# Kernel tuning notes

Hardware: AMD Instinct MI355X
Metric: run time of the kernel (lower is better)

The kernel has to match this reference:

```python
import jax, jax.numpy as jnp
import numpy as np

N_NODES = 20000
N_EDGES = 320000
IN_CH = 512
HID = 128
HEADS = 4
OUT_CH = 30
NEG_SLOPE = 0.2  # PyG GATConv default negative_slope


def add_self_loops(ei, n):
    loops = jnp.arange(n, dtype=ei.dtype)
    return jnp.concatenate([ei, jnp.stack([loops, loops])], axis=1)


def gat_layer(x, ei, W, a_src, a_dst, b, concat):
    # x: [N, F_in], ei: [2, E] (source row 0 -> target row 1), W: [F_in, H*C]
    n = x.shape[0]
    H, C = a_src.shape
    h = (x @ W).reshape(n, H, C)                      # [N, H, C]
    src, dst = ei[0], ei[1]
    al_src = jnp.einsum('nhc,hc->nh', h, a_src)       # [N, H]
    al_dst = jnp.einsum('nhc,hc->nh', h, a_dst)
    e = al_src[src] + al_dst[dst]                     # [E, H]
    e = jnp.where(e > 0, e, NEG_SLOPE * e)            # LeakyReLU
    # segment softmax over destination nodes (stable)
    emax = jax.lax.stop_gradient(jax.ops.segment_max(e, dst, num_segments=n))
    p = jnp.exp(e - emax[dst])
    denom = jax.ops.segment_sum(p, dst, num_segments=n)
    alpha = p / denom[dst]                            # [E, H]
    msg = h[src] * alpha[:, :, None]                  # [E, H, C]
    out = jax.ops.segment_sum(msg, dst, num_segments=n)  # [N, H, C]
    out = out.reshape(n, H * C) if concat else out.mean(axis=1)
    return out + b


def setup_inputs() -> dict:
    key = jax.random.key(0)
    ks = jax.random.split(key, 12)
    s = 0.05
    x = jax.random.normal(ks[0], (N_NODES, IN_CH), jnp.float32)
    edge_index = jax.random.randint(ks[1], (2, N_EDGES), 0, N_NODES, jnp.int32)
    return {
        'x': x,
        'edge_index': edge_index,
        'W1': jax.random.normal(ks[2], (IN_CH, HEADS * HID), jnp.float32) * s,
        'a_src1': jax.random.normal(ks[3], (HEADS, HID), jnp.float32) * s,
        'a_dst1': jax.random.normal(ks[4], (HEADS, HID), jnp.float32) * s,
        'b1': jnp.zeros((HEADS * HID,), jnp.float32),
        'W2': jax.random.normal(ks[5], (HEADS * HID, OUT_CH), jnp.float32) * s,
        'a_src2': jax.random.normal(ks[6], (1, OUT_CH), jnp.float32) * s,
        'a_dst2': jax.random.normal(ks[7], (1, OUT_CH), jnp.float32) * s,
        'b2': jnp.zeros((OUT_CH,), jnp.float32),
        'Wd': jax.random.normal(ks[8], (OUT_CH, IN_CH), jnp.float32) * s,
        'bd': jnp.zeros((IN_CH,), jnp.float32),
    }


def reference(x, edge_index, W1, a_src1, a_dst1, b1, W2, a_src2, a_dst2, b2, Wd, bd):
    n = x.shape[0]
    ei = add_self_loops(edge_index, n)
    h = gat_layer(x, ei, W1, a_src1, a_dst1, b1, concat=True)   # [N, HEADS*HID]
    h = jax.nn.elu(h)                                           # dropout is identity in eval
    z = gat_layer(h, ei, W2, a_src2, a_dst2, b2, concat=False)  # [N, OUT_CH]
    x_hat = z @ Wd + bd                                         # [N, IN_CH]
    return (x_hat, z)
```

## Files before the change

kernel.cpp:

```cpp
#include <hip/hip_runtime.h>
#include <hip/hip_bf16.h>
#include <stdint.h>

#define N_NODES 20000
#define N_EDGES 320000
#define IN_CH 512
#define HID 128
#define HEADS 4
#define HC 512
#define OUT_CH 30
#define NEG_SLOPE 0.2f
#define M_PAD 20096

typedef _Float16 half8 __attribute__((ext_vector_type(8)));
typedef _Float16 half4v __attribute__((ext_vector_type(4)));
typedef float f32x4 __attribute__((ext_vector_type(4)));

static __device__ __forceinline__ float lrelu(float e) { return e > 0.f ? e : NEG_SLOPE * e; }

static __device__ __forceinline__ void gload16(const void* gsrc, void* ldst) {
  __builtin_amdgcn_global_load_lds(
      (const __attribute__((address_space(1))) uint32_t*)gsrc,
      (__attribute__((address_space(3))) uint32_t*)ldst,
      16, 0, 0);
}

__global__ __launch_bounds__(256) void k_cast_x(const float* __restrict__ x,
                                                _Float16* __restrict__ xh,
                                                int* __restrict__ cnt) {
  int i = blockIdx.x * blockDim.x + threadIdx.x;
  if (i < N_NODES) cnt[i] = 0;
  int base = i * 4;
  int row = base >> 9;
  half4v o;
  if (row < N_NODES) {
    float4 v = *(const float4*)(x + (size_t)base);
    o[0] = (_Float16)v.x; o[1] = (_Float16)v.y; o[2] = (_Float16)v.z; o[3] = (_Float16)v.w;
  } else {
    o[0] = o[1] = o[2] = o[3] = (_Float16)0.f;
  }
  *(half4v*)(xh + (size_t)base) = o;
}

__global__ __launch_bounds__(256) void k_prep_w(const float* __restrict__ W1,
                                                const float* __restrict__ W2,
                                                _Float16* __restrict__ W1t,
                                                _Float16* __restrict__ w2t) {
  __shared__ float t[64][65];
  const int b = blockIdx.x;
  const int tid = threadIdx.x;
  if (b < 64) {
    const int bk = (b & 7) * 64;
    const int bn = (b >> 3) * 64;
#pragma unroll
    for (int it = 0; it < 16; it++) {
      int idx = tid + it * 256;
      int r = idx >> 6, c = idx & 63;
      t[r][c] = W1[(size_t)(bk + r) * HC + bn + c];
    }
    __syncthreads();
#pragma unroll
    for (int it = 0; it < 16; it++) {
      int idx = tid + it * 256;
      int rn = idx >> 6, ck = idx & 63;
      W1t[(size_t)(bn + rn) * IN_CH + bk + ck] = (_Float16)t[ck][rn];
    }
  } else {
    int idx = (b - 64) * 256 + tid;
    int n = idx >> 9, k = idx & 511;
    w2t[idx] = (n < OUT_CH) ? (_Float16)W2[(size_t)k * OUT_CH + n] : (_Float16)0.f;
  }
}

__global__ __launch_bounds__(256) void k_gemm1_mfma(const _Float16* __restrict__ A,
                                                    const _Float16* __restrict__ Bt,
                                                    _Float16* __restrict__ C,
                                                    const float* __restrict__ a_src,
                                                    const float* __restrict__ a_dst,
                                                    float* __restrict__ al_s,
                                                    float* __restrict__ al_d) {
  __shared__ _Float16 smem[128 * 136];
  _Float16* As = smem;
  _Float16* Bs = smem + 128 * 64;
  _Float16* Cs = smem;
  const int tid = threadIdx.x;
  const int lane = tid & 63;
  const int w = tid >> 6;
  const int bm = blockIdx.x * 128;
  const int bn = blockIdx.y * 128;

  const int lrow = lane >> 3;
  const int schunk = (lane & 7) ^ lrow;

  const int wm = w >> 1, wn = w & 1;
  const int r15 = lane & 15;
  const int q = lane >> 4;
  const int a_row0 = wm * 64 + r15;
  const int b_row0 = wn * 64 + r15;

  f32x4 acc[4][4];
  const f32x4 zero = {0.f, 0.f, 0.f, 0.f};
#pragma unroll
  for (int i = 0; i < 4; i++)
#pragma unroll
    for (int j = 0; j < 4; j++) acc[i][j] = zero;

  for (int kb = 0; kb < 8; kb++) {
    const int kof = kb * 64 + schunk * 8;
#pragma unroll
    for (int t = 0; t < 4; t++) {
      const int row = w * 32 + t * 8;
      gload16(A + (size_t)(bm + row + lrow) * IN_CH + kof, (void*)(As + row * 64));
      gload16(Bt + (size_t)(bn + row + lrow) * IN_CH + kof, (void*)(Bs + row * 64));
    }
    __syncthreads();
#pragma unroll
    for (int s = 0; s < 2; s++) {
      const int cs = ((s * 4 + q) ^ (lane & 7)) * 8;
      half8 af[4], bf[4];
#pragma unroll
      for (int i = 0; i < 4; i++) af[i] = *(const half8*)&As[(a_row0 + i * 16) * 64 + cs];
#pragma unroll
      for (int j = 0; j < 4; j++) bf[j] = *(const half8*)&Bs[(b_row0 + j * 16) * 64 + cs];
#pragma unroll
      for (int i = 0; i < 4; i++)
#pragma unroll
        for (int j = 0; j < 4; j++)
          acc[i][j] = __builtin_amdgcn_mfma_f32_16x16x32_f16(af[i], bf[j], acc[i][j], 0, 0, 0);
    }
    __syncthreads();
  }
#pragma unroll
  for (int i = 0; i < 4; i++)
#pragma unroll
    for (int j = 0; j < 4; j++)
#pragma unroll
      for (int r = 0; r < 4; r++) {
        const int row = wm * 64 + i * 16 + q * 4 + r;
        const int col = wn * 64 + j * 16 + r15;
        Cs[row * 136 + col] = (_Float16)acc[i][j][r];
      }
  __syncthreads();
#pragma unroll
  for (int it = 0; it < 8; it++) {
    int cidx = tid + it * 256;
    int row = cidx >> 4, c16 = cidx & 15;
    int gm = bm + row;
    if (gm < N_NODES)
      *(half8*)(C + (size_t)gm * HC + bn + c16 * 8) = *(const half8*)&Cs[row * 136 + c16 * 8];
  }
  const int head = blockIdx.y;
  const int row = tid >> 1;
  const int hf = tid & 1;
  const float* asp = a_src + head * HID + hf * 64;
  const float* adp = a_dst + head * HID + hf * 64;
  float s = 0.f, d = 0.f;
#pragma unroll
  for (int j8 = 0; j8 < 8; j8++) {
    half8 cv = *(const half8*)&Cs[row * 136 + hf * 64 + j8 * 8];
    float4 a0 = *(const float4*)(asp + j8 * 8);
    float4 a1 = *(const float4*)(asp + j8 * 8 + 4);
    float4 d0 = *(const float4*)(adp + j8 * 8);
    float4 d1 = *(const float4*)(adp + j8 * 8 + 4);
    float c0 = (float)cv[0], c1 = (float)cv[1], c2 = (float)cv[2], c3 = (float)cv[3];
    float c4 = (float)cv[4], c5 = (float)cv[5], c6 = (float)cv[6], c7 = (float)cv[7];
    s += c0 * a0.x + c1 * a0.y + c2 * a0.z + c3 * a0.w +
         c4 * a1.x + c5 * a1.y + c6 * a1.z + c7 * a1.w;
    d += c0 * d0.x + c1 * d0.y + c2 * d0.z + c3 * d0.w +
         c4 * d1.x + c5 * d1.y + c6 * d1.z + c7 * d1.w;
  }
  s += __shfl_xor(s, 1);
  d += __shfl_xor(d, 1);
  const int gm = bm + row;
  if (hf == 0 && gm < N_NODES) {
    al_s[gm * HEADS + head] = s;
    al_d[gm * HEADS + head] = d;
  }
}

#define PARTS 79
__global__ void k_count(const int* __restrict__ dst, int* __restrict__ cnt) {
  int e = blockIdx.x * blockDim.x + threadIdx.x;
  if (e < N_EDGES) atomicAdd(&cnt[dst[e]], 1);
}
__global__ __launch_bounds__(256) void k_scan_part(const int* __restrict__ cnt,
                                                   int* __restrict__ part) {
  __shared__ int ws[4];
  int i = blockIdx.x * 256 + threadIdx.x;
  int v = (i < N_NODES) ? cnt[i] : 0;
  int lane = threadIdx.x & 63;
#pragma unroll
  for (int off = 32; off; off >>= 1) v += __shfl_down(v, off);
  if (lane == 0) ws[threadIdx.x >> 6] = v;
  __syncthreads();
  if (threadIdx.x == 0) part[blockIdx.x] = ws[0] + ws[1] + ws[2] + ws[3];
}
__global__ __launch_bounds__(128) void k_scan_tops(int* __restrict__ part,
                                                   int* __restrict__ offs) {
  __shared__ int buf[128];
  int t = threadIdx.x;
  int v = (t < PARTS) ? part[t] : 0;
  buf[t] = v;
  __syncthreads();
#pragma unroll
  for (int off = 1; off < 128; off <<= 1) {
    int x = (t >= off) ? buf[t - off] : 0;
    __syncthreads();
    buf[t] += x;
    __syncthreads();
  }
  if (t < PARTS) part[t] = buf[t] - v;
  if (t == PARTS - 1) offs[N_NODES] = buf[t];
}
__global__ __launch_bounds__(256) void k_scan_final(const int* __restrict__ cnt,
                                                    const int* __restrict__ part,
                                                    int* __restrict__ offs,
                                                    int* __restrict__ cursor) {
  __shared__ int buf[256];
  int i = blockIdx.x * 256 + threadIdx.x;
  int t = threadIdx.x;
  int v = (i < N_NODES) ? cnt[i] : 0;
  buf[t] = v;
  __syncthreads();
#pragma unroll
  for (int off = 1; off < 256; off <<= 1) {
    int x = (t >= off) ? buf[t - off] : 0;
    __syncthreads();
    buf[t] += x;
    __syncthreads();
  }
  if (i < N_NODES) {
    int ex = part[blockIdx.x] + buf[t] - v;
    offs[i] = ex;
    cursor[i] = ex;
  }
}
__global__ void k_scatter(const int* __restrict__ src, const int* __restrict__ dst,
                          int* __restrict__ cursor, int* __restrict__ srcs) {
  int e = blockIdx.x * blockDim.x + threadIdx.x;
  if (e < N_EDGES) {
    int pos = atomicAdd(&cursor[dst[e]], 1);
    srcs[pos] = src[e];
  }
}

__global__ __launch_bounds__(256) void k_agg1(const _Float16* __restrict__ h,
                                              const float* __restrict__ al_s,
                                              const float* __restrict__ al_d,
                                              const int* __restrict__ offs,
                                              const int* __restrict__ srcs,
                                              const float* __restrict__ b1,
                                              _Float16* __restrict__ hm) {
  const int lane = threadIdx.x & 63;
  const int qq = lane >> 4;
  const int l16 = lane & 15;
  const int head = blockIdx.x / 1250;
  const int n = (blockIdx.x % 1250) * 16 + (threadIdx.x >> 6) * 4 + qq;
  const int cb = head * HID + l16 * 8;

  const float adn = al_d[n * HEADS + head];
  const float pself = __expf(lrelu(al_s[n * HEADS + head] + adn));

  half8 hv = *(const half8*)(h + (size_t)n * HC + cb);
  float acc[8];
  float den = pself;
#pragma unroll
  for (int j = 0; j < 8; j++) acc[j] = pself * (float)hv[j];

  const int beg = offs[n];
  const int cnt = offs[n + 1] - beg;
  int mx = cnt;
  mx = max(mx, __shfl_xor(mx, 16));
  mx = max(mx, __shfl_xor(mx, 32));
  const int kb = qq * 16;

  for (int base = 0; base < mx; base += 16) {
    int sreg = n;
    float preg = 0.f;
    if (base + l16 < cnt) {
      sreg = srcs[beg + base + l16];
      preg = __expf(lrelu(al_s[sreg * HEADS + head] + adn));
    }
    int m = min(16, cnt - base);
    int m4 = (m + 3) & ~3;
    for (int k = 0; k < m4; k += 4) {
      int s0 = __shfl(sreg, kb + k);
      int s1 = __shfl(sreg, kb + k + 1);
      int s2 = __shfl(sreg, kb + k + 2);
      int s3 = __shfl(sreg, kb + k + 3);
      float p0 = __shfl(preg, kb + k);
      float p1 = __shfl(preg, kb + k + 1);
      float p2 = __shfl(preg, kb + k + 2);
      float p3 = __shfl(preg, kb + k + 3);
      half8 v0 = *(const half8*)(h + (size_t)s0 * HC + cb);
      half8 v1 = *(const half8*)(h + (size_t)s1 * HC + cb);
      half8 v2 = *(const half8*)(h + (size_t)s2 * HC + cb);
      half8 v3 = *(const half8*)(h + (size_t)s3 * HC + cb);
      den += p0 + p1 + p2 + p3;
#pragma unroll
      for (int j = 0; j < 8; j++)
        acc[j] += p0 * (float)v0[j] + p1 * (float)v1[j] +
                  p2 * (float)v2[j] + p3 * (float)v3[j];
    }
  }
  const float inv = 1.f / den;
  float4 bb0 = *(const float4*)(b1 + cb);
  float4 bb1 = *(const float4*)(b1 + cb + 4);
  float ob[8] = {bb0.x, bb0.y, bb0.z, bb0.w, bb1.x, bb1.y, bb1.z, bb1.w};
  half8 ov;
#pragma unroll
  for (int j = 0; j < 8; j++) {
    float o = acc[j] * inv + ob[j];
    o = o > 0.f ? o : __expf(o) - 1.f;
    ov[j] = (_Float16)o;
  }
  *(half8*)(hm + (size_t)n * HC + cb) = ov;
}

__global__ __launch_bounds__(256) void k_gemm2_mfma(const _Float16* __restrict__ hm,
                                                    const _Float16* __restrict__ w2t,
                                                    const float* __restrict__ a_s2,
                                                    const float* __restrict__ a_d2,
                                                    float* __restrict__ zpre,
                                                    float* __restrict__ al_s2,
                                                    float* __restrict__ al_d2) {
  __shared__ _Float16 Bs[32 * 520];
  __shared__ _Float16 As[64 * 136];
  const int tid = threadIdx.x;
  const int lane = tid & 63;
  const int w = tid >> 6;
  const int bm = blockIdx.x * 64;
  const int n15 = lane & 15;
  const int q = lane >> 4;

#pragma unroll
  for (int it = 0; it < 8; it++) {
    int idx = (tid + it * 256) * 8;
    int n = idx >> 9, k = idx & 511;
    *(half8*)&Bs[n * 520 + k] = *(const half8*)(w2t + idx);
  }

  f32x4 acc0 = {0.f, 0.f, 0.f, 0.f}, acc1 = {0.f, 0.f, 0.f, 0.f};
  for (int kt = 0; kt < HC; kt += 128) {
#pragma unroll
    for (int p = 0; p < 4; p++) {
      int row = (tid >> 4) + p * 16;
      int kof = (tid & 15) * 8;
      int gm = bm + row;
      half8 v = {};
      if (gm < N_NODES) v = *(const half8*)(hm + (size_t)gm * HC + kt + kof);
      *(half8*)&As[row * 136 + kof] = v;
    }
    __syncthreads();
#pragma unroll
    for (int ks = 0; ks < 128; ks += 32) {
      half8 af = *(const half8*)&As[(w * 16 + n15) * 136 + ks + q * 8];
      half8 b0 = *(const half8*)&Bs[n15 * 520 + kt + ks + q * 8];
      half8 b1 = *(const half8*)&Bs[(16 + n15) * 520 + kt + ks + q * 8];
      acc0 = __builtin_amdgcn_mfma_f32_16x16x32_f16(af, b0, acc0, 0, 0, 0);
      acc1 = __builtin_amdgcn_mfma_f32_16x16x32_f16(af, b1, acc1, 0, 0, 0);
    }
    __syncthreads();
  }
  const float asn0 = (n15 < OUT_CH) ? a_s2[n15] : 0.f;
  const float asn1 = (n15 + 16 < OUT_CH) ? a_s2[n15 + 16] : 0.f;
  const float adn0 = (n15 < OUT_CH) ? a_d2[n15] : 0.f;
  const float adn1 = (n15 + 16 < OUT_CH) ? a_d2[n15 + 16] : 0.f;
#pragma unroll
  for (int r = 0; r < 4; r++) {
    const int gm = bm + w * 16 + q * 4 + r;
    const bool ok = gm < N_NODES;
    if (ok) {
      zpre[(size_t)gm * OUT_CH + n15] = acc0[r];
      if (n15 + 16 < OUT_CH) zpre[(size_t)gm * OUT_CH + n15 + 16] = acc1[r];
    }
    float s = acc0[r] * asn0 + acc1[r] * asn1;
    float d = acc0[r] * adn0 + acc1[r] * adn1;
#pragma unroll
    for (int off = 8; off; off >>= 1) {
      s += __shfl_xor(s, off);
      d += __shfl_xor(d, off);
    }
    if (n15 == 0 && ok) {
      al_s2[gm] = s;
      al_d2[gm] = d;
    }
  }
}

__global__ __launch_bounds__(256) void k_agg2(const float* __restrict__ zpre,
                                              const float* __restrict__ al_s2,
                                              const float* __restrict__ al_d2,
                                              const int* __restrict__ offs,
                                              const int* __restrict__ srcs,
                                              const float* __restrict__ b2,
                                              float* __restrict__ zout) {
  const int lane = threadIdx.x & 63;
  const int hh = lane >> 5;
  const int l32 = lane & 31;
  const int n = blockIdx.x * 8 + (threadIdx.x >> 6) * 2 + hh;
  const float ad2n = al_d2[n];
  const float pself = __expf(lrelu(al_s2[n] + ad2n));
  const bool act = l32 < OUT_CH;
  float zv = act ? zpre[(size_t)n * OUT_CH + l32] : 0.f;
  float acc = pself * zv;
  float den = pself;

  const int beg = offs[n];
  const int cnt = offs[n + 1] - beg;
  int mx = max(cnt, __shfl_xor(cnt, 32));
  const int kb = hh * 32;

  for (int base = 0; base < mx; base += 32) {
    int sreg = n;
    float preg = 0.f;
    if (base + l32 < cnt) {
      sreg = srcs[beg + base + l32];
      preg = __expf(lrelu(al_s2[sreg] + ad2n));
    }
    int m = min(32, cnt - base);
    int m4 = (m + 3) & ~3;
    for (int k = 0; k < m4; k += 4) {
      int s0 = __shfl(sreg, kb + k);
      int s1 = __shfl(sreg, kb + k + 1);
      int s2 = __shfl(sreg, kb + k + 2);
      int s3 = __shfl(sreg, kb + k + 3);
      float p0 = __shfl(preg, kb + k);
      float p1 = __shfl(preg, kb + k + 1);
      float p2 = __shfl(preg, kb + k + 2);
      float p3 = __shfl(preg, kb + k + 3);
      float v0 = act ? zpre[(size_t)s0 * OUT_CH + l32] : 0.f;
      float v1 = act ? zpre[(size_t)s1 * OUT_CH + l32] : 0.f;
      float v2 = act ? zpre[(size_t)s2 * OUT_CH + l32] : 0.f;
      float v3 = act ? zpre[(size_t)s3 * OUT_CH + l32] : 0.f;
      den += p0 + p1 + p2 + p3;
      acc += p0 * v0 + p1 * v1 + p2 * v2 + p3 * v3;
    }
  }
  if (act) zout[(size_t)n * OUT_CH + l32] = acc / den + b2[l32];
}

__global__ __launch_bounds__(256) void k_dec(const float* __restrict__ z,
                                             const float* __restrict__ Wd,
                                             const float* __restrict__ bd,
                                             float* __restrict__ xhat) {
  __shared__ float zs[64][32];
  const int tid = threadIdx.x;
  const int c = blockIdx.y * 256 + tid;
  float wd[32];
#pragma unroll
  for (int k = 0; k < OUT_CH; k++) wd[k] = Wd[(size_t)k * IN_CH + c];
  wd[30] = wd[31] = 0.f;
  const int n0 = blockIdx.x * 64;
  for (int idx = tid; idx < 64 * 32; idx += 256) {
    int r = idx >> 5, cc = idx & 31;
    int row = n0 + r;
    zs[r][cc] = (cc < OUT_CH && row < N_NODES) ? z[(size_t)row * OUT_CH + cc] : 0.f;
  }
  __syncthreads();
  const float b0 = bd[c];
  for (int i = 0; i < 64; i++) {
    int row = n0 + i;
    if (row >= N_NODES) break;
    float a0 = b0;
#pragma unroll
    for (int k4 = 0; k4 < 8; k4++) {
      float4 zv = *(const float4*)&zs[i][k4 * 4];
      a0 += zv.x * wd[k4 * 4 + 0] + zv.y * wd[k4 * 4 + 1] +
            zv.z * wd[k4 * 4 + 2] + zv.w * wd[k4 * 4 + 3];
    }
    xhat[(size_t)row * IN_CH + c] = a0;
  }
}

extern "C" void kernel_launch(void* const* d_in, const int* in_sizes, int n_in,
                              void* d_out, int out_size, void* d_ws, size_t ws_size,
                              hipStream_t stream) {
  const float* x    = (const float*)d_in[0];
  const int*   ei   = (const int*)d_in[1];
  const float* W1   = (const float*)d_in[2];
  const float* a_s1 = (const float*)d_in[3];
  const float* a_d1 = (const float*)d_in[4];
  const float* b1   = (const float*)d_in[5];
  const float* W2   = (const float*)d_in[6];
  const float* a_s2 = (const float*)d_in[7];
  const float* a_d2 = (const float*)d_in[8];
  const float* b2   = (const float*)d_in[9];
  const float* Wd   = (const float*)d_in[10];
  const float* bd   = (const float*)d_in[11];

  float* xhat = (float*)d_out;
  float* zout = xhat + (size_t)N_NODES * IN_CH;

  const int* srcv = ei;
  const int* dstv = ei + N_EDGES;

  char* w = (char*)d_ws;
  auto alloc = [&](size_t bytes) {
    void* p = (void*)w;
    w += (bytes + 255) & ~(size_t)255;
    return p;
  };
  _Float16* xh   = (_Float16*)alloc((size_t)M_PAD * IN_CH * 2);
  _Float16* w1t  = (_Float16*)alloc((size_t)HC * IN_CH * 2);
  _Float16* w2t  = (_Float16*)alloc((size_t)32 * HC * 2);
  _Float16* h    = (_Float16*)alloc((size_t)N_NODES * HC * 2);
  _Float16* hm   = (_Float16*)alloc((size_t)N_NODES * HC * 2);
  float* zpre  = (float*)alloc((size_t)N_NODES * OUT_CH * 4);
  float* al_s1v= (float*)alloc((size_t)N_NODES * HEADS * 4);
  float* al_d1v= (float*)alloc((size_t)N_NODES * HEADS * 4);
  float* al_s2v= (float*)alloc((size_t)N_NODES * 4);
  float* al_d2v= (float*)alloc((size_t)N_NODES * 4);
  int*   cnt   = (int*)alloc((size_t)N_NODES * 4);
  int*   offs  = (int*)alloc((size_t)(N_NODES + 1) * 4);
  int*   cursor= (int*)alloc((size_t)N_NODES * 4);
  int*   srcs  = (int*)alloc((size_t)N_EDGES * 4);
  int*   part  = (int*)alloc((size_t)PARTS * 4);

  const int EB = (N_EDGES + 255) / 256;

  k_prep_w<<<128, 256, 0, stream>>>(W1, W2, w1t, w2t);
  k_cast_x<<<M_PAD * IN_CH / 4 / 256, 256, 0, stream>>>(x, xh, cnt);
  k_gemm1_mfma<<<dim3(M_PAD / 128, HC / 128), 256, 0, stream>>>(xh, w1t, h, a_s1, a_d1,
                                                                al_s1v, al_d1v);
  k_count<<<EB, 256, 0, stream>>>(dstv, cnt);
  k_scan_part<<<PARTS, 256, 0, stream>>>(cnt, part);
  k_scan_tops<<<1, 128, 0, stream>>>(part, offs);
  k_scan_final<<<PARTS, 256, 0, stream>>>(cnt, part, offs, cursor);
  k_scatter<<<EB, 256, 0, stream>>>(srcv, dstv, cursor, srcs);
  k_agg1<<<1250 * HEADS, 256, 0, stream>>>(h, al_s1v, al_d1v, offs, srcs, b1, hm);
  k_gemm2_mfma<<<(N_NODES + 63) / 64, 256, 0, stream>>>(hm, w2t, a_s2, a_d2, zpre,
                                                        al_s2v, al_d2v);
  k_agg2<<<N_NODES / 8, 256, 0, stream>>>(zpre, al_s2v, al_d2v, offs, srcs, b2, zout);
  k_dec<<<dim3((N_NODES + 63) / 64, 2), 256, 0, stream>>>(zout, Wd, bd, xhat);
}
```

Measured before the change: 267.0 us.

## Merge front kernels, fold edge count into GEMM1, drop scan_tops, LDS edge staging

Merges the x cast and weight prep into a single launch and appends the edge-count atomics as extra blocks of the GEMM1 grid, so both run in one dispatch. Removes the single-block top-level scan by having each final-scan block sum the earlier partials itself. In both aggregation kernels, source indices and weights are staged in LDS and read back as vector loads, replacing eight cross-lane shuffles per four edges. The goal is fewer launches and fewer serialized tiny kernels. The cost is some redundant partial summation and extra LDS traffic.

```diff
diff --git a/kernel.cpp b/kernel.cpp
--- a/kernel.cpp
+++ b/kernel.cpp
@@ -11,6 +11,10 @@
 #define OUT_CH 30
 #define NEG_SLOPE 0.2f
 #define M_PAD 20096
+#define PARTS 79
+#define CAST_BLOCKS (M_PAD * IN_CH / 4 / 256)
+#define G1_BLOCKS (M_PAD / 128 * 4)
+#define CNT_BLOCKS (N_EDGES / 256)
 
 typedef _Float16 half8 __attribute__((ext_vector_type(8)));
 typedef _Float16 half4v __attribute__((ext_vector_type(4)));
@@ -25,33 +29,33 @@
       16, 0, 0);
 }
 
-__global__ __launch_bounds__(256) void k_cast_x(const float* __restrict__ x,
-                                                _Float16* __restrict__ xh,
-                                                int* __restrict__ cnt) {
-  int i = blockIdx.x * blockDim.x + threadIdx.x;
-  if (i < N_NODES) cnt[i] = 0;
-  int base = i * 4;
-  int row = base >> 9;
-  half4v o;
-  if (row < N_NODES) {
-    float4 v = *(const float4*)(x + (size_t)base);
-    o[0] = (_Float16)v.x; o[1] = (_Float16)v.y; o[2] = (_Float16)v.z; o[3] = (_Float16)v.w;
-  } else {
-    o[0] = o[1] = o[2] = o[3] = (_Float16)0.f;
-  }
-  *(half4v*)(xh + (size_t)base) = o;
-}
-
-__global__ __launch_bounds__(256) void k_prep_w(const float* __restrict__ W1,
-                                                const float* __restrict__ W2,
-                                                _Float16* __restrict__ W1t,
-                                                _Float16* __restrict__ w2t) {
+__global__ __launch_bounds__(256) void k_front(const float* __restrict__ x,
+                                               const float* __restrict__ W1,
+                                               const float* __restrict__ W2,
+                                               _Float16* __restrict__ xh,
+                                               _Float16* __restrict__ W1t,
+                                               _Float16* __restrict__ w2t,
+                                               int* __restrict__ cnt) {
   __shared__ float t[64][65];
   const int b = blockIdx.x;
   const int tid = threadIdx.x;
-  if (b < 64) {
-    const int bk = (b & 7) * 64;
-    const int bn = (b >> 3) * 64;
+  if (b < CAST_BLOCKS) {
+    int i = b * 256 + tid;
+    if (i < N_NODES) cnt[i] = 0;
+    int base = i * 4;
+    int row = base >> 9;
+    half4v o;
+    if (row < N_NODES) {
+      float4 v = *(const float4*)(x + (size_t)base);
+      o[0] = (_Float16)v.x; o[1] = (_Float16)v.y; o[2] = (_Float16)v.z; o[3] = (_Float16)v.w;
+    } else {
+      o[0] = o[1] = o[2] = o[3] = (_Float16)0.f;
+    }
+    *(half4v*)(xh + (size_t)base) = o;
+  } else if (b < CAST_BLOCKS + 64) {
+    const int bb = b - CAST_BLOCKS;
+    const int bk = (bb & 7) * 64;
+    const int bn = (bb >> 3) * 64;
 #pragma unroll
     for (int it = 0; it < 16; it++) {
       int idx = tid + it * 256;
@@ -66,7 +70,7 @@
       W1t[(size_t)(bn + rn) * IN_CH + bk + ck] = (_Float16)t[ck][rn];
     }
   } else {
-    int idx = (b - 64) * 256 + tid;
+    int idx = (b - CAST_BLOCKS - 64) * 256 + tid;
     int n = idx >> 9, k = idx & 511;
     w2t[idx] = (n < OUT_CH) ? (_Float16)W2[(size_t)k * OUT_CH + n] : (_Float16)0.f;
   }
@@ -78,16 +82,25 @@
                                                     const float* __restrict__ a_src,
                                                     const float* __restrict__ a_dst,
                                                     float* __restrict__ al_s,
-                                                    float* __restrict__ al_d) {
+                                                    float* __restrict__ al_d,
+                                                    const int* __restrict__ dst,
+                                                    int* __restrict__ cnt) {
   __shared__ _Float16 smem[128 * 136];
+  const int bx = blockIdx.x;
+  const int tid = threadIdx.x;
+  if (bx >= G1_BLOCKS) {
+    int e = (bx - G1_BLOCKS) * 256 + tid;
+    if (e < N_EDGES) atomicAdd(&cnt[dst[e]], 1);
+    return;
+  }
   _Float16* As = smem;
   _Float16* Bs = smem + 128 * 64;
   _Float16* Cs = smem;
-  const int tid = threadIdx.x;
   const int lane = tid & 63;
   const int w = tid >> 6;
-  const int bm = blockIdx.x * 128;
-  const int bn = blockIdx.y * 128;
+  const int bm = (bx >> 2) * 128;
+  const int head = bx & 3;
+  const int bn = head * 128;
 
   const int lrow = lane >> 3;
   const int schunk = (lane & 7) ^ lrow;
@@ -149,7 +162,6 @@
     if (gm < N_NODES)
       *(half8*)(C + (size_t)gm * HC + bn + c16 * 8) = *(const half8*)&Cs[row * 136 + c16 * 8];
   }
-  const int head = blockIdx.y;
   const int row = tid >> 1;
   const int hf = tid & 1;
   const float* asp = a_src + head * HID + hf * 64;
@@ -178,11 +190,6 @@
   }
 }
 
-#define PARTS 79
-__global__ void k_count(const int* __restrict__ dst, int* __restrict__ cnt) {
-  int e = blockIdx.x * blockDim.x + threadIdx.x;
-  if (e < N_EDGES) atomicAdd(&cnt[dst[e]], 1);
-}
 __global__ __launch_bounds__(256) void k_scan_part(const int* __restrict__ cnt,
                                                    int* __restrict__ part) {
   __shared__ int ws[4];
@@ -195,30 +202,22 @@
   __syncthreads();
   if (threadIdx.x == 0) part[blockIdx.x] = ws[0] + ws[1] + ws[2] + ws[3];
 }
-__global__ __launch_bounds__(128) void k_scan_tops(int* __restrict__ part,
-                                                   int* __restrict__ offs) {
-  __shared__ int buf[128];
-  int t = threadIdx.x;
-  int v = (t < PARTS) ? part[t] : 0;
-  buf[t] = v;
-  __syncthreads();
-#pragma unroll
-  for (int off = 1; off < 128; off <<= 1) {
-    int x = (t >= off) ? buf[t - off] : 0;
-    __syncthreads();
-    buf[t] += x;
-    __syncthreads();
-  }
-  if (t < PARTS) part[t] = buf[t] - v;
-  if (t == PARTS - 1) offs[N_NODES] = buf[t];
-}
 __global__ __launch_bounds__(256) void k_scan_final(const int* __restrict__ cnt,
                                                     const int* __restrict__ part,
                                                     int* __restrict__ offs,
                                                     int* __restrict__ cursor) {
   __shared__ int buf[256];
-  int i = blockIdx.x * 256 + threadIdx.x;
-  int t = threadIdx.x;
+  __shared__ int s_prefix;
+  const int b = blockIdx.x;
+  const int t = threadIdx.x;
+  if (t < 64) {
+    int v = 0;
+    for (int j = t; j < b; j += 64) v += part[j];
+#pragma unroll
+    for (int off = 32; off; off >>= 1) v += __shfl_down(v, off);
+    if (t == 0) s_prefix = v;
+  }
+  int i = b * 256 + t;
   int v = (i < N_NODES) ? cnt[i] : 0;
   buf[t] = v;
   __syncthreads();
@@ -230,10 +229,11 @@
     __syncthreads();
   }
   if (i < N_NODES) {
-    int ex = part[blockIdx.x] + buf[t] - v;
+    int ex = s_prefix + buf[t] - v;
     offs[i] = ex;
     cursor[i] = ex;
   }
+  if (b == PARTS - 1 && t == 255) offs[N_NODES] = s_prefix + buf[255];
 }
 __global__ void k_scatter(const int* __restrict__ src, const int* __restrict__ dst,
                           int* __restrict__ cursor, int* __restrict__ srcs) {
@@ -251,11 +251,14 @@
                                               const int* __restrict__ srcs,
                                               const float* __restrict__ b1,
                                               _Float16* __restrict__ hm) {
-  const int lane = threadIdx.x & 63;
+  __shared__ __align__(16) int2 s_sp[4][64];
+  const int tid = threadIdx.x;
+  const int lane = tid & 63;
+  const int wv = tid >> 6;
   const int qq = lane >> 4;
   const int l16 = lane & 15;
   const int head = blockIdx.x / 1250;
-  const int n = (blockIdx.x % 1250) * 16 + (threadIdx.x >> 6) * 4 + qq;
+  const int n = (blockIdx.x % 1250) * 16 + wv * 4 + qq;
   const int cb = head * HID + l16 * 8;
 
   const float adn = al_d[n * HEADS + head];
@@ -272,7 +275,6 @@
   int mx = cnt;
   mx = max(mx, __shfl_xor(mx, 16));
   mx = max(mx, __shfl_xor(mx, 32));
-  const int kb = qq * 16;
 
   for (int base = 0; base < mx; base += 16) {
     int sreg = n;
@@ -281,27 +283,26 @@
       sreg = srcs[beg + base + l16];
       preg = __expf(lrelu(al_s[sreg * HEADS + head] + adn));
     }
-    int m = min(16, cnt - base);
-    int m4 = (m + 3) & ~3;
+    s_sp[wv][lane] = make_int2(sreg, __float_as_int(preg));
+    __builtin_amdgcn_wave_barrier();
+    const int rem = cnt - base;
+    const int m4 = rem > 16 ? 16 : ((rem + 3) & ~3);
     for (int k = 0; k < m4; k += 4) {
-      int s0 = __shfl(sreg, kb + k);
-      int s1 = __shfl(sreg, kb + k + 1);
-      int s2 = __shfl(sreg, kb + k + 2);
-      int s3 = __shfl(sreg, kb + k + 3);
-      float p0 = __shfl(preg, kb + k);
-      float p1 = __shfl(preg, kb + k + 1);
-      float p2 = __shfl(preg, kb + k + 2);
-      float p3 = __shfl(preg, kb + k + 3);
-      half8 v0 = *(const half8*)(h + (size_t)s0 * HC + cb);
-      half8 v1 = *(const half8*)(h + (size_t)s1 * HC + cb);
-      half8 v2 = *(const half8*)(h + (size_t)s2 * HC + cb);
-      half8 v3 = *(const half8*)(h + (size_t)s3 * HC + cb);
+      int4 w0 = *(const int4*)&s_sp[wv][qq * 16 + k];
+      int4 w1 = *(const int4*)&s_sp[wv][qq * 16 + k + 2];
+      half8 v0 = *(const half8*)(h + (size_t)w0.x * HC + cb);
+      half8 v1 = *(const half8*)(h + (size_t)w0.z * HC + cb);
+      half8 v2 = *(const half8*)(h + (size_t)w1.x * HC + cb);
+      half8 v3 = *(const half8*)(h + (size_t)w1.z * HC + cb);
+      float p0 = __int_as_float(w0.y), p1 = __int_as_float(w0.w);
+      float p2 = __int_as_float(w1.y), p3 = __int_as_float(w1.w);
       den += p0 + p1 + p2 + p3;
 #pragma unroll
       for (int j = 0; j < 8; j++)
         acc[j] += p0 * (float)v0[j] + p1 * (float)v1[j] +
                   p2 * (float)v2[j] + p3 * (float)v3[j];
     }
+    __builtin_amdgcn_wave_barrier();
   }
   const float inv = 1.f / den;
   float4 bb0 = *(const float4*)(b1 + cb);
@@ -395,10 +396,13 @@
                                               const int* __restrict__ srcs,
                                               const float* __restrict__ b2,
                                               float* __restrict__ zout) {
-  const int lane = threadIdx.x & 63;
+  __shared__ __align__(16) int2 s_sp[4][64];
+  const int tid = threadIdx.x;
+  const int lane = tid & 63;
+  const int wv = tid >> 6;
   const int hh = lane >> 5;
   const int l32 = lane & 31;
-  const int n = blockIdx.x * 8 + (threadIdx.x >> 6) * 2 + hh;
+  const int n = blockIdx.x * 8 + wv * 2 + hh;
   const float ad2n = al_d2[n];
   const float pself = __expf(lrelu(al_s2[n] + ad2n));
   const bool act = l32 < OUT_CH;
@@ -409,7 +413,6 @@
   const int beg = offs[n];
   const int cnt = offs[n + 1] - beg;
   int mx = max(cnt, __shfl_xor(cnt, 32));
-  const int kb = hh * 32;
 
   for (int base = 0; base < mx; base += 32) {
     int sreg = n;
@@ -418,24 +421,23 @@
       sreg = srcs[beg + base + l32];
       preg = __expf(lrelu(al_s2[sreg] + ad2n));
     }
-    int m = min(32, cnt - base);
-    int m4 = (m + 3) & ~3;
+    s_sp[wv][lane] = make_int2(sreg, __float_as_int(preg));
+    __builtin_amdgcn_wave_barrier();
+    const int rem = cnt - base;
+    const int m4 = rem > 32 ? 32 : ((rem + 3) & ~3);
     for (int k = 0; k < m4; k += 4) {
-      int s0 = __shfl(sreg, kb + k);
-      int s1 = __shfl(sreg, kb + k + 1);
-      int s2 = __shfl(sreg, kb + k + 2);
-      int s3 = __shfl(sreg, kb + k + 3);
-      float p0 = __shfl(preg, kb + k);
-      float p1 = __shfl(preg, kb + k + 1);
-      float p2 = __shfl(preg, kb + k + 2);
-      float p3 = __shfl(preg, kb + k + 3);
-      float v0 = act ? zpre[(size_t)s0 * OUT_CH + l32] : 0.f;
-      float v1 = act ? zpre[(size_t)s1 * OUT_CH + l32] : 0.f;
-      float v2 = act ? zpre[(size_t)s2 * OUT_CH + l32] : 0.f;
-      float v3 = act ? zpre[(size_t)s3 * OUT_CH + l32] : 0.f;
+      int4 w0 = *(const int4*)&s_sp[wv][hh * 32 + k];
+      int4 w1 = *(const int4*)&s_sp[wv][hh * 32 + k + 2];
+      float v0 = act ? zpre[(size_t)w0.x * OUT_CH + l32] : 0.f;
+      float v1 = act ? zpre[(size_t)w0.z * OUT_CH + l32] : 0.f;
+      float v2 = act ? zpre[(size_t)w1.x * OUT_CH + l32] : 0.f;
+      float v3 = act ? zpre[(size_t)w1.z * OUT_CH + l32] : 0.f;
+      float p0 = __int_as_float(w0.y), p1 = __int_as_float(w0.w);
+      float p2 = __int_as_float(w1.y), p3 = __int_as_float(w1.w);
       den += p0 + p1 + p2 + p3;
       acc += p0 * v0 + p1 * v1 + p2 * v2 + p3 * v3;
     }
+    __builtin_amdgcn_wave_barrier();
   }
   if (act) zout[(size_t)n * OUT_CH + l32] = acc / den + b2[l32];
 }
@@ -519,13 +521,10 @@
 
   const int EB = (N_EDGES + 255) / 256;
 
-  k_prep_w<<<128, 256, 0, stream>>>(W1, W2, w1t, w2t);
-  k_cast_x<<<M_PAD * IN_CH / 4 / 256, 256, 0, stream>>>(x, xh, cnt);
-  k_gemm1_mfma<<<dim3(M_PAD / 128, HC / 128), 256, 0, stream>>>(xh, w1t, h, a_s1, a_d1,
-                                                                al_s1v, al_d1v);
-  k_count<<<EB, 256, 0, stream>>>(dstv, cnt);
+  k_front<<<CAST_BLOCKS + 128, 256, 0, stream>>>(x, W1, W2, xh, w1t, w2t, cnt);
+  k_gemm1_mfma<<<G1_BLOCKS + CNT_BLOCKS, 256, 0, stream>>>(xh, w1t, h, a_s1, a_d1,
+                                                           al_s1v, al_d1v, dstv, cnt);
   k_scan_part<<<PARTS, 256, 0, stream>>>(cnt, part);
-  k_scan_tops<<<1, 128, 0, stream>>>(part, offs);
   k_scan_final<<<PARTS, 256, 0, stream>>>(cnt, part, offs, cursor);
   k_scatter<<<EB, 256, 0, stream>>>(srcv, dstv, cursor, srcs);
   k_agg1<<<1250 * HEADS, 256, 0, stream>>>(h, al_s1v, al_d1v, offs, srcs, b1, hm);
```

Result: faster. 256.4 us (-4.0%).
